# Kernel tuning notes

Hardware: AMD Instinct MI355X
Metric: run time of the kernel (lower is better)

The kernel has to match this reference:

```python
import jax, jax.numpy as jnp
import numpy as np

L_IN, L_FREQ, L_OUT = 128, 64, 64
C_IN, C_OUT, T_DIM = 64, 64, 256
SPIN = 1

# ---------- self-contained spin-weighted SHT (MW sampling), replacing s2fft ----------

def _mw_thetas(L, extended):
    n = 2 * L - 1 if extended else L
    return (2 * np.arange(n) + 1) * np.pi / (2 * L - 1)

def _wigner_d_stack(L, thetas, n):
    # d^l_{m,n}(theta) = <l,m| exp(-i theta Jy) |l,n>, computed via eigh of the
    # Hermitian angular-momentum operator Jy. Output (ntheta, L, 2L-1), m at col L-1+m.
    nth = len(thetas)
    out = np.zeros((nth, L, 2 * L - 1), dtype=np.float64)
    for l in range(abs(n), L):
        dim = 2 * l + 1
        m = np.arange(-l, l).astype(np.float64)
        ap = np.sqrt(l * (l + 1.0) - m * (m + 1.0))
        Jy = np.zeros((dim, dim), dtype=np.complex128)
        i = np.arange(dim - 1)
        Jy[i + 1, i] = -0.5j * ap
        Jy[i, i + 1] = 0.5j * ap
        lam, V = np.linalg.eigh(Jy)
        coeff = V * np.conj(V[l + n, :])[None, :]
        phases = np.exp(-1j * np.outer(lam, thetas))
        out[:, l, L - 1 - l:L + l] = (coeff @ phases).T.real
    return out

def _mw_quad_weights(L):
    # per-theta weights on the mirror-extended grid: q_t = (1/(2L-1)) sum_k w(k) e^{ik theta_t}
    # with w(k) = int_0^pi e^{ik t} sin(t) dt
    k = np.arange(-(L - 1), L)
    den = np.where(np.abs(k) == 1, 1, 1 - k * k).astype(np.float64)
    w = np.where(k % 2 == 0, 2.0 / den, 0.0).astype(np.complex128)
    w[k == 1] = 0.5j * np.pi
    w[k == -1] = -0.5j * np.pi
    th = _mw_thetas(L, True)
    return ((w[None, :] * np.exp(1j * np.outer(th, k))).sum(1) / (2 * L - 1)).real

# transform kernels are constants (built once at import, numpy)
_D_FWD = jnp.asarray(_wigner_d_stack(L_IN, _mw_thetas(L_IN, True), -SPIN) * _mw_quad_weights(L_IN)[:, None, None], jnp.float32)
_D_INV = jnp.asarray(_wigner_d_stack(L_OUT, _mw_thetas(L_OUT, False), -SPIN), jnp.float32)
_CL_IN = jnp.asarray(((-1.0) ** SPIN) * np.sqrt((2 * np.arange(L_IN) + 1) / (4 * np.pi)), jnp.float32)
_CL_OUT = jnp.asarray(((-1.0) ** SPIN) * np.sqrt((2 * np.arange(L_OUT) + 1) / (4 * np.pi)), jnp.float32)
_m_all = np.arange(-(L_IN - 1), L_IN)
_PARITY = jnp.asarray(np.where((_m_all + SPIN) % 2 == 0, 1.0, -1.0), jnp.float32)

def sht_forward(x):
    # x: (L_IN, 2*L_IN-1, C) real spatial -> flm: (L_IN, 2*L_IN-1, C) complex, m at L_IN-1+m
    nphi = 2 * L_IN - 1
    ftm = jnp.fft.fftshift(jnp.fft.fft(x, axis=1), axes=1) * (2 * jnp.pi / nphi)
    # mirror extension in theta with (-1)^(m+spin) parity (all channels at once)
    g_ext = jnp.concatenate([ftm, _PARITY[None, :, None] * ftm[::-1][1:]], axis=0)
    flm = jnp.einsum('tlm,tmc->lmc', _D_FWD, g_ext)
    return flm * _CL_IN[:, None, None]

def sht_inverse(flm):
    # flm: (L_OUT, 2*L_OUT-1, C) complex -> (L_OUT, 2*L_OUT-1, C) real spatial
    ftm = jnp.einsum('tlm,lmc->tmc', _D_INV, flm * _CL_OUT[:, None, None])
    return (jnp.fft.ifft(jnp.fft.ifftshift(ftm, axes=1), axis=1) * (2 * L_OUT - 1)).real

def resize_flm(flm, l_in, l_out):
    # centered truncation / zero-pad of (L, 2L-1, C) harmonic coefficients
    if l_out <= l_in:
        d = l_in - l_out
        return flm[:l_out, d:d + 2 * l_out - 1]
    d = l_out - l_in
    return jnp.pad(flm, ((0, d), (d, d), (0, 0)))

# ---------- inputs and parameters ----------

def setup_inputs():
    key = jax.random.key(0)
    ks = jax.random.split(key, 12)
    n = lambda i, shape, s: jax.random.normal(ks[i], shape, jnp.float32) * s
    return {
        'x': jax.random.normal(ks[0], (L_IN, 2 * L_IN - 1, C_IN), jnp.float32),
        't_emb': jax.random.normal(ks[1], (T_DIM,), jnp.float32),
        'spec_conv_w': n(2, (C_IN, C_OUT), (1.0 / C_IN) ** 0.5),
        'spec_conv_b': jnp.zeros((C_OUT,), jnp.float32),
        'spec_wr': n(3, (L_FREQ, C_IN, C_OUT), (0.5 / C_IN) ** 0.5),
        'spec_wi': n(4, (L_FREQ, C_IN, C_OUT), (0.5 / C_IN) ** 0.5),
        'spec_tr_w': n(5, (T_DIM, L_FREQ), (1.0 / T_DIM) ** 0.5),
        'spec_tr_b': jnp.zeros((L_FREQ,), jnp.float32),
        'spec_ti_w': n(6, (T_DIM, L_FREQ), (1.0 / T_DIM) ** 0.5),
        'spec_ti_b': jnp.zeros((L_FREQ,), jnp.float32),
        'spat_conv1_w': n(7, (C_IN, C_OUT), (1.0 / C_IN) ** 0.5),
        'spat_conv1_b': jnp.zeros((C_OUT,), jnp.float32),
        'spat_t_w': n(8, (T_DIM, 2 * C_OUT), (1.0 / T_DIM) ** 0.5),
        'spat_t_b': jnp.zeros((2 * C_OUT,), jnp.float32),
        'spat_weight': n(9, (C_OUT, C_OUT), 0.01),
        'spat_conv2_w': n(10, (C_OUT, C_OUT), (1.0 / C_OUT) ** 0.5),
        'spat_conv2_b': jnp.zeros((C_OUT,), jnp.float32),
        'ln_scale': jnp.ones((C_OUT,), jnp.float32),
        'ln_bias': jnp.zeros((C_OUT,), jnp.float32),
    }

def reference(x, t_emb, spec_conv_w, spec_conv_b, spec_wr, spec_wi, spec_tr_w, spec_tr_b, spec_ti_w, spec_ti_b, spat_conv1_w, spat_conv1_b, spat_t_w, spat_t_b, spat_weight, spat_conv2_w, spat_conv2_b, ln_scale, ln_bias):
    # ----- SphericalSpectralTimeConv branch -----
    flm = sht_forward(x)                                   # (L_IN, 2L_IN-1, C_IN) complex
    flm = resize_flm(flm, L_IN, L_FREQ)                    # (L_FREQ, 2L_FREQ-1, C_IN)
    conv_flm = jnp.einsum('lmi,io->lmo', flm, spec_conv_w) + spec_conv_b
    t_c = (t_emb @ spec_tr_w + spec_tr_b) + 1j * (t_emb @ spec_ti_w + spec_ti_b)   # (L_FREQ,)
    w = t_c[:, None, None] * (spec_wr + 1j * spec_wi)      # (L_FREQ, C_IN, C_OUT)
    flm = jnp.einsum('lmi,lio->lmo', flm, w) + conv_flm
    xs = sht_inverse(resize_flm(flm, L_FREQ, L_OUT))       # (L_OUT, 2L_OUT-1, C_OUT) real
    xs = xs / (jnp.linalg.norm(xs, axis=-1, keepdims=True) + 1e-6)
    # ----- SpatialTimeConv branch (path='down') -----
    h = jnp.einsum('lmi,io->lmo', x, spat_conv1_w) + spat_conv1_b
    t = t_emb @ spat_t_w + spat_t_b
    w_t, b_t = t[:C_OUT], t[C_OUT:]
    h = jnp.einsum('lmi,io->lmo', h, w_t[None, :] * spat_weight)
    h = sht_inverse(resize_flm(sht_forward(h), L_IN, L_OUT))
    h = jnp.einsum('lmi,io->lmo', h, spat_conv2_w) + spat_conv2_b + b_t
    # ----- combine: add, gelu, LayerNorm (eps=1e-6 over channels) -----
    y = jax.nn.gelu(xs + h)
    mu = jnp.mean(y, axis=-1, keepdims=True)
    var = jnp.var(y, axis=-1, keepdims=True)
    return (y - mu) * jax.lax.rsqrt(var + 1e-6) * ln_scale + ln_bias
```

## Files before the change

### kernel.cpp

```cpp
#include <hip/hip_runtime.h>
#include <math.h>

#define DPI 3.141592653589793238462643383279502884

__device__ __forceinline__ float wave_sum64(float v) {
#pragma unroll
  for (int off = 32; off > 0; off >>= 1) v += __shfl_xor(v, off, 64);
  return v;
}

__device__ __forceinline__ float gelu_tanh(float v) {
  float u = 0.7978845608028654f * (v + 0.044715f * v * v * v);
  return 0.5f * v * (1.0f + tanhf(u));
}

#define CN255F ((float)(-2.0 * DPI / 255.0))
#define CN127F ((float)(2.0 * DPI / 127.0))


__device__ __forceinline__ void dft_block(int idx, int tid, const float* __restrict__ x,
                                          float* __restrict__ Are, float* __restrict__ Aim,
                                          float* __restrict__ Bre, float* __restrict__ Bim,
                                          char* sm) {
  float* xs_ = (float*)sm;
  int t = idx >> 1, ph = idx & 1;
  float* ore = ph ? Bre : Are;
  float* oim = ph ? Bim : Aim;
  int pbase = ph * 128;
  int Ktot = ph ? 127 : 128;
  int cg_ = tid & 15, mg = tid >> 4;
  float wr[4], wi[4], rc[4], rs[4];
#pragma unroll
  for (int j = 0; j < 4; ++j) {
    int m = mg * 4 + j;
    __sincosf(CN255F * (float)m, &rs[j], &rc[j]);
    int r0 = (m * pbase) % 255;
    __sincosf(CN255F * (float)r0, &wi[j], &wr[j]);
  }
  float accr[4][4], acci[4][4];
#pragma unroll
  for (int j = 0; j < 4; ++j)
#pragma unroll
    for (int q = 0; q < 4; ++q) { accr[j][q] = 0.f; acci[j][q] = 0.f; }
  for (int k0 = 0; k0 < Ktot; k0 += 64) {
    int kn = (Ktot - k0 < 64) ? Ktot - k0 : 64;
    __syncthreads();
    {
      const float4* src = (const float4*)(x + ((size_t)t * 255 + pbase + k0) * 64);
      float4* dst = (float4*)xs_;
      int lim = kn * 16;
#pragma unroll
      for (int q = 0; q < 4; ++q) {
        int fidx = tid + q * 256;
        if (fidx < lim) dst[fidx] = src[fidx];
      }
    }
    __syncthreads();
#pragma unroll 2
    for (int k = 0; k < kn; ++k) {
      float4 xv = *(const float4*)&xs_[k * 64 + cg_ * 4];
      float xv4[4] = {xv.x, xv.y, xv.z, xv.w};
#pragma unroll
      for (int j = 0; j < 4; ++j) {
#pragma unroll
        for (int q = 0; q < 4; ++q) {
          accr[j][q] = fmaf(xv4[q], wr[j], accr[j][q]);
          acci[j][q] = fmaf(xv4[q], wi[j], acci[j][q]);
        }
        float nw = wr[j] * rc[j] - wi[j] * rs[j];
        wi[j] = fmaf(wr[j], rs[j], wi[j] * rc[j]);
        wr[j] = nw;
      }
    }
  }
#pragma unroll
  for (int j = 0; j < 4; ++j) {
    int mi = mg * 4 + j;
    size_t ob = ((size_t)t * 64 + mi) * 64 + cg_ * 4;
    *(float4*)(ore + ob) = make_float4(accr[j][0], accr[j][1], accr[j][2], accr[j][3]);
    *(float4*)(oim + ob) = make_float4(acci[j][0], acci[j][1], acci[j][2], acci[j][3]);
  }
}

__device__ __forceinline__ void wigner_block(int wb, int tid, float* __restrict__ Deff,
                                             float* __restrict__ Dinv, char* sm) {
  float* LF = (float*)sm;
  double* red = (double*)(sm + 512);
  float* clf = (float*)(sm + 1024);
  int mode = (wb < 128) ? 0 : 1;
  int t, mm;
  if (mode == 0) { t = wb; mm = tid; }
  else { mm = wb - 128; t = (tid < 64) ? tid : 63; }
  if (tid < 64) clf[tid] = (float)(-sqrt((2.0 * tid + 1.0) / (4.0 * DPI)));
  if (tid < 128) LF[tid] = (tid == 0) ? 0.f : logf((float)tid);
  __syncthreads();
  for (int s = 1; s < 128; s <<= 1) {
    float add = (tid < 128 && tid >= s) ? LF[tid - s] : 0.f;
    __syncthreads();
    if (tid < 128) LF[tid] += add;
    __syncthreads();
  }
  double denomN = (mode == 0) ? 255.0 : 127.0;
  double beta = (2.0 * t + 1.0) * DPI / denomN;
  float coeff = 1.0f;
  if (mode == 0) {
    if (tid < 63) {
      int k = 2 * (tid + 1);
      red[tid] = 8.0 * cos((double)k * beta) / (1.0 - (double)k * (double)k);
    } else if (tid == 63) {
      red[63] = 4.0;
    }
    __syncthreads();
    for (int s = 32; s > 0; s >>= 1) {
      if (tid < s) red[tid] += red[tid + s];
      __syncthreads();
    }
    double s = red[0] / 255.0;
    if (t == 127) s *= 0.5;
    coeff = (float)(s * (2.0 * DPI / 255.0));
  }
  bool active = (mode == 0) ? (tid < 127) : (tid < 64);
  if (!active) return;
  int m = mm - 63;
  double chd, shd;
  sincos(0.5 * beta, &shd, &chd);
  float cbf = (float)cos(beta);
  float chf = (float)chd, shf = (float)shd;
  int am = (m < 0) ? -m : m;
  int l0v = (am > 1) ? am : 1;
  float seed;
  if (m == 0) {
    seed = -1.4142135623730951f * shf * chf;
  } else {
    int j = am;
    float lch = logf(chf), lsh = logf(shf);
    float e0 = 0.5f * (LF[2 * j] - LF[j - 1] - LF[j + 1]);
    float expo = (m >= 1) ? e0 + (float)(j - 1) * lch + (float)(j + 1) * lsh
                          : e0 + (float)(j + 1) * lch + (float)(j - 1) * lsh;
    float sv = __expf(expo);
    seed = (m >= 1 && ((m + 1) & 1)) ? -sv : sv;
  }
  float dl = seed, dm1 = 0.0f, S_cur = 0.0f;
  float mf = (float)m;
  for (int l = 0; l < 64; ++l) {
    float val = 0.0f;
    if (l >= l0v) {
      val = dl * coeff * clf[l];
      float Ld = (float)l, lp = Ld + 1.0f;
      float S_next = sqrtf((lp * lp - mf * mf) * (lp * lp - 1.0f));
      float num1 = (2.0f * Ld + 1.0f) * (Ld * lp * cbf + mf);
      float dn = (num1 * dl - lp * S_cur * dm1) / (Ld * S_next);
      dm1 = dl; dl = dn; S_cur = S_next;
    }
    if (mode == 0) Deff[((size_t)t * 127 + mm) * 64 + l] = val;
    else Dinv[((size_t)mm * 64 + l) * 64 + t] = val;
  }
}

__device__ __forceinline__ void a2_block(int l, int tid, const float* __restrict__ temb,
                                         const float* __restrict__ trw, const float* __restrict__ trb,
                                         const float* __restrict__ tiw, const float* __restrict__ tib,
                                         const float* __restrict__ scw, const float* __restrict__ swr,
                                         const float* __restrict__ swi, float2* __restrict__ A2,
                                         char* sm) {
  float* fb1 = (float*)sm;
  float* fb2 = (float*)(sm + 1024);
  fb1[tid] = temb[tid] * trw[tid * 64 + l];
  fb2[tid] = temb[tid] * tiw[tid * 64 + l];
  __syncthreads();
  for (int s = 128; s > 0; s >>= 1) {
    if (tid < s) { fb1[tid] += fb1[tid + s]; fb2[tid] += fb2[tid + s]; }
    __syncthreads();
  }
  float tr = fb1[0] + trb[l], ti = fb2[0] + tib[l];
  int o = tid & 63, iq = tid >> 6;
  for (int i = iq * 16; i < iq * 16 + 16; ++i) {
    int idx = (l * 64 + i) * 64 + o;
    float r = swr[idx], s2 = swi[idx];
    A2[idx] = make_float2(scw[i * 64 + o] + tr * r - ti * s2, tr * s2 + ti * r);
  }
}

__device__ __forceinline__ void m_block(int j, int tid, const float* __restrict__ temb,
                                        const float* __restrict__ stw, const float* __restrict__ stb,
                                        const float* __restrict__ c1w, const float* __restrict__ c1b,
                                        const float* __restrict__ sweight, float* __restrict__ Mm,
                                        float* __restrict__ bias2, char* sm) {
  float* fb1 = (float*)sm;
  float* fb2 = (float*)(sm + 1024);
  int o = tid & 63, part = tid >> 6;
  float p = 0.f;
  for (int k = part * 64; k < part * 64 + 64; ++k)
    p = fmaf(temb[k], stw[k * 128 + o], p);
  fb1[part * 64 + o] = p;
  __syncthreads();
  if (part == 0) fb2[o] = fb1[o] + fb1[64 + o] + fb1[128 + o] + fb1[192 + o] + stb[o];
  __syncthreads();
  float tvo = fb2[o];
  float q = 0.f;
  for (int i = part * 16; i < part * 16 + 16; ++i)
    q = fmaf(c1w[j * 64 + i], sweight[i * 64 + o], q);
  __syncthreads();
  fb1[part * 64 + o] = q;
  __syncthreads();
  if (part == 0) Mm[j * 64 + o] = tvo * (fb1[o] + fb1[64 + o] + fb1[128 + o] + fb1[192 + o]);
  if (j == 0) {
    float bq = 0.f;
    for (int i = part * 16; i < part * 16 + 16; ++i)
      bq = fmaf(c1b[i], sweight[i * 64 + o], bq);
    __syncthreads();
    fb1[part * 64 + o] = bq;
    __syncthreads();
    if (part == 0) bias2[o] = tvo * (fb1[o] + fb1[64 + o] + fb1[128 + o] + fb1[192 + o]);
  }
}

__device__ __forceinline__ void tv_block(int tid, const float* __restrict__ temb,
                                         const float* __restrict__ stw, const float* __restrict__ stb,
                                         float* __restrict__ tv, char* sm) {
  float* fb1 = (float*)sm;
  int o = tid & 127, part = tid >> 7;
  float p = 0.f;
  for (int k = part * 128; k < part * 128 + 128; ++k)
    p = fmaf(temb[k], stw[k * 128 + o], p);
  fb1[part * 128 + o] = p;
  __syncthreads();
  if (part == 0) tv[o] = fb1[o] + fb1[128 + o] + stb[o];
}

__global__ __launch_bounds__(256) void ct_pre(
    const float* __restrict__ x, const float* __restrict__ temb,
    const float* __restrict__ trw, const float* __restrict__ trb,
    const float* __restrict__ tiw, const float* __restrict__ tib,
    const float* __restrict__ stw, const float* __restrict__ stb,
    const float* __restrict__ scw, const float* __restrict__ swr,
    const float* __restrict__ swi, const float* __restrict__ c1w,
    const float* __restrict__ c1b, const float* __restrict__ sweight,
    float* __restrict__ Deff, float* __restrict__ Dinv,
    float2* __restrict__ A2, float* __restrict__ Mm,
    float* __restrict__ bias2, float* __restrict__ tv,
    float* __restrict__ ftmA_re, float* __restrict__ ftmA_im,
    float* __restrict__ ftmB_re, float* __restrict__ ftmB_im) {
  __shared__ __align__(16) char sm[16384];
  int vb = blockIdx.x;
  int tid = threadIdx.x;
  if (vb < 255) wigner_block(vb, tid, Deff, Dinv, sm);
  else if (vb < 319) a2_block(vb - 255, tid, temb, trw, trb, tiw, tib, scw, swr, swi, A2, sm);
  else if (vb < 383) m_block(vb - 319, tid, temb, stw, stb, c1w, c1b, sweight, Mm, bias2, sm);
  else if (vb < 384) tv_block(tid, temb, stw, stb, tv, sm);
  else dft_block(vb - 384, tid, x, ftmA_re, ftmA_im, ftmB_re, ftmB_im, sm);
}

__global__ __launch_bounds__(256) void ct_projf(const float* __restrict__ Deff,
                                                const float* __restrict__ fAre,
                                                const float* __restrict__ fAim,
                                                const float* __restrict__ fBre,
                                                const float* __restrict__ fBim,
                                                float* __restrict__ flmA_re, float* __restrict__ flmA_im,
                                                float* __restrict__ flmB_re, float* __restrict__ flmB_im) {
  __shared__ float Dsh[64][32];
  __shared__ float fr_[64][64], fi_[64][64];
  int mm = blockIdx.x, lh = blockIdx.y, th = blockIdx.z;
  float* ore = th ? flmB_re : flmA_re;
  float* oim = th ? flmB_im : flmA_im;
  int tb = th * 64;
  int mi = (mm >= 63) ? (mm - 63) : (63 - mm);
  float csign = (mm >= 63) ? 1.0f : -1.0f;
  int tid = threadIdx.x;
  int cg_ = tid & 15, lg = tid >> 4;
  for (int e = tid; e < 64 * 32; e += 256) {
    int r = e >> 5, li = e & 31;
    Dsh[r][li] = Deff[((size_t)(tb + r) * 127 + mm) * 64 + lh * 32 + li];
  }
  for (int e = tid; e < 64 * 64; e += 256) {
    int r = e >> 6, c = e & 63;
    size_t idx = ((size_t)(tb + r) * 64 + mi) * 64 + c;
    fr_[r][c] = fAre[idx] + fBre[idx];
    fi_[r][c] = csign * (fAim[idx] + fBim[idx]);
  }
  __syncthreads();
  float ar[2][4], ai[2][4];
#pragma unroll
  for (int li = 0; li < 2; ++li)
#pragma unroll
    for (int q = 0; q < 4; ++q) { ar[li][q] = 0.f; ai[li][q] = 0.f; }
#pragma unroll 4
  for (int k = 0; k < 64; ++k) {
    float4 fr4 = *(const float4*)&fr_[k][cg_ * 4];
    float4 fi4 = *(const float4*)&fi_[k][cg_ * 4];
    float2 d2 = *(const float2*)&Dsh[k][lg * 2];
    float frv[4] = {fr4.x, fr4.y, fr4.z, fr4.w};
    float fiv[4] = {fi4.x, fi4.y, fi4.z, fi4.w};
    float dv[2] = {d2.x, d2.y};
#pragma unroll
    for (int li = 0; li < 2; ++li)
#pragma unroll
      for (int q = 0; q < 4; ++q) {
        ar[li][q] = fmaf(dv[li], frv[q], ar[li][q]);
        ai[li][q] = fmaf(dv[li], fiv[q], ai[li][q]);
      }
  }
#pragma unroll
  for (int li = 0; li < 2; ++li) {
    size_t row = ((size_t)mm * 64 + lh * 32 + lg * 2 + li) * 64 + cg_ * 4;
    *(float4*)(ore + row) = make_float4(ar[li][0], ar[li][1], ar[li][2], ar[li][3]);
    *(float4*)(oim + row) = make_float4(ai[li][0], ai[li][1], ai[li][2], ai[li][3]);
  }
}

__global__ __launch_bounds__(256) void ct_mix(const float* __restrict__ flmA_re,
                                              const float* __restrict__ flmA_im,
                                              const float* __restrict__ flmB_re,
                                              const float* __restrict__ flmB_im,
                                              const float2* __restrict__ A2,
                                              const float* __restrict__ Mm,
                                              const float* __restrict__ scb,
                                              const float* __restrict__ bias2,
                                              const float* __restrict__ Deff,
                                              float* __restrict__ s_re, float* __restrict__ s_im,
                                              float* __restrict__ h_re, float* __restrict__ h_im) {
  __shared__ float Ar_[64][32], Ai_[64][32], Msh[64][32];
  __shared__ float Br_[64][65], Bi_[64][65];
  __shared__ float rb[256];
  int l = blockIdx.x, mh = blockIdx.y, oh = blockIdx.z;
  int tid = threadIdx.x;
  int og = tid & 15, mg = tid >> 4;
  rb[tid] = (mh == 0 && tid < 128) ? Deff[((size_t)tid * 127 + 63) * 64 + l] : 0.f;
  __syncthreads();
  for (int s = 128; s > 0; s >>= 1) {
    if (tid < s) rb[tid] += rb[tid + s];
    __syncthreads();
  }
  float slv = rb[0];
  for (int e = tid; e < 64 * 32; e += 256) {
    int r = e >> 5, oi = e & 31;
    float2 aa = A2[((size_t)l * 64 + r) * 64 + oh * 32 + oi];
    Ar_[r][oi] = aa.x; Ai_[r][oi] = aa.y;
    Msh[r][oi] = Mm[r * 64 + oh * 32 + oi];
  }
  for (int e = tid; e < 64 * 64; e += 256) {
    int mi = e >> 6, i = e & 63;
    int gmm = mh * 64 + mi; if (gmm > 126) gmm = 126;
    size_t idx = ((size_t)gmm * 64 + l) * 64 + i;
    Br_[mi][i] = flmA_re[idx] + flmB_re[idx];
    Bi_[mi][i] = flmA_im[idx] + flmB_im[idx];
  }
  __syncthreads();
  int o0 = oh * 32 + og * 2;
  float b0[2] = {scb[o0], scb[o0 + 1]};
  float sr[4][2], si[4][2], hr[4][2], hi[4][2];
#pragma unroll
  for (int jm = 0; jm < 4; ++jm)
#pragma unroll
    for (int qo = 0; qo < 2; ++qo) {
      sr[jm][qo] = b0[qo]; si[jm][qo] = 0.f; hr[jm][qo] = 0.f; hi[jm][qo] = 0.f;
    }
#pragma unroll 4
  for (int k = 0; k < 64; ++k) {
    float2 ar2 = *(const float2*)&Ar_[k][og * 2];
    float2 ai2 = *(const float2*)&Ai_[k][og * 2];
    float2 mv2 = *(const float2*)&Msh[k][og * 2];
    float br4[4], bi4[4];
#pragma unroll
    for (int jm = 0; jm < 4; ++jm) {
      br4[jm] = Br_[mg * 4 + jm][k];
      bi4[jm] = Bi_[mg * 4 + jm][k];
    }
    float arv[2] = {ar2.x, ar2.y}, aiv[2] = {ai2.x, ai2.y}, mvv[2] = {mv2.x, mv2.y};
#pragma unroll
    for (int jm = 0; jm < 4; ++jm)
#pragma unroll
      for (int qo = 0; qo < 2; ++qo) {
        sr[jm][qo] = fmaf(br4[jm], arv[qo], sr[jm][qo]);
        sr[jm][qo] = fmaf(-bi4[jm], aiv[qo], sr[jm][qo]);
        si[jm][qo] = fmaf(br4[jm], aiv[qo], si[jm][qo]);
        si[jm][qo] = fmaf(bi4[jm], arv[qo], si[jm][qo]);
        hr[jm][qo] = fmaf(br4[jm], mvv[qo], hr[jm][qo]);
        hi[jm][qo] = fmaf(bi4[jm], mvv[qo], hi[jm][qo]);
      }
  }
  float bb[2] = {bias2[o0], bias2[o0 + 1]};
#pragma unroll
  for (int jm = 0; jm < 4; ++jm) {
    int gmm = mh * 64 + mg * 4 + jm;
    if (gmm > 126) continue;
    if (gmm == 63) {
#pragma unroll
      for (int qo = 0; qo < 2; ++qo)
        hr[jm][qo] = fmaf(255.0f * slv, bb[qo], hr[jm][qo]);
    }
    size_t row = ((size_t)gmm * 64 + l) * 64 + o0;
    *(float2*)(s_re + row) = make_float2(sr[jm][0], sr[jm][1]);
    *(float2*)(s_im + row) = make_float2(si[jm][0], si[jm][1]);
    *(float2*)(h_re + row) = make_float2(hr[jm][0], hr[jm][1]);
    *(float2*)(h_im + row) = make_float2(hi[jm][0], hi[jm][1]);
  }
}

__global__ __launch_bounds__(256) void ct_proji(const float* __restrict__ Dinv,
                                                const float* __restrict__ s_re,
                                                const float* __restrict__ s_im,
                                                const float* __restrict__ h_re,
                                                const float* __restrict__ h_im,
                                                float* __restrict__ fos_re, float* __restrict__ fos_im,
                                                float* __restrict__ foh_re, float* __restrict__ foh_im) {
  __shared__ float Dsh[64][64];
  __shared__ float Br_[64][32], Bi_[64][32];
  int mm = blockIdx.x, br = blockIdx.y, ch = blockIdx.z;
  const float* ire = br ? h_re : s_re;
  const float* iim = br ? h_im : s_im;
  float* ore = br ? foh_re : fos_re;
  float* oim = br ? foh_im : fos_im;
  int tid = threadIdx.x;
  int cg_ = tid & 15, tg = tid >> 4;
  for (int e = tid; e < 64 * 64; e += 256) {
    int r = e >> 6, tt = e & 63;
    Dsh[r][tt] = Dinv[((size_t)mm * 64 + r) * 64 + tt];
  }
  for (int e = tid; e < 64 * 32; e += 256) {
    int r = e >> 5, cc = e & 31;
    size_t idx = ((size_t)mm * 64 + r) * 64 + ch * 32 + cc;
    Br_[r][cc] = ire[idx];
    Bi_[r][cc] = iim[idx];
  }
  __syncthreads();
  float ar[4][2], ai[4][2];
#pragma unroll
  for (int j = 0; j < 4; ++j)
#pragma unroll
    for (int q = 0; q < 2; ++q) { ar[j][q] = 0.f; ai[j][q] = 0.f; }
#pragma unroll 4
  for (int k = 0; k < 64; ++k) {
    float4 d4 = *(const float4*)&Dsh[k][tg * 4];
    float2 fr2 = *(const float2*)&Br_[k][cg_ * 2];
    float2 fi2 = *(const float2*)&Bi_[k][cg_ * 2];
    float dv[4] = {d4.x, d4.y, d4.z, d4.w};
    float frv[2] = {fr2.x, fr2.y}, fiv[2] = {fi2.x, fi2.y};
#pragma unroll
    for (int j = 0; j < 4; ++j)
#pragma unroll
      for (int q = 0; q < 2; ++q) {
        ar[j][q] = fmaf(dv[j], frv[q], ar[j][q]);
        ai[j][q] = fmaf(dv[j], fiv[q], ai[j][q]);
      }
  }
#pragma unroll
  for (int j = 0; j < 4; ++j) {
    int t = tg * 4 + j;
    size_t ob = ((size_t)t * 127 + mm) * 64 + ch * 32 + cg_ * 2;
    *(float2*)(ore + ob) = make_float2(ar[j][0], ar[j][1]);
    *(float2*)(oim + ob) = make_float2(ai[j][0], ai[j][1]);
  }
}

__global__ __launch_bounds__(256) void ct_idft(const float* __restrict__ fos_re,
                                               const float* __restrict__ fos_im,
                                               const float* __restrict__ foh_re,
                                               const float* __restrict__ foh_im,
                                               float* __restrict__ xsbA, float* __restrict__ xsbB,
                                               float* __restrict__ hsbA, float* __restrict__ hsbB) {
  __shared__ float Br_[32][64], Bi_[32][64];
  int t = blockIdx.x, br = blockIdx.y;
  int z = blockIdx.z;
  int ph = z >> 1, kh = z & 1;
  const float* fre = br ? foh_re : fos_re;
  const float* fim = br ? foh_im : fos_im;
  float* outp = br ? (kh ? hsbB : hsbA) : (kh ? xsbB : xsbA);
  int kbase = kh * 64;
  int Ktot = kh ? 63 : 64;
  int tid = threadIdx.x;
  int cg_ = tid & 15, pg = tid >> 4;
  float wc[4], ws[4], rc[4], rs[4];
#pragma unroll
  for (int j = 0; j < 4; ++j) {
    int gp = ph * 64 + pg * 4 + j; if (gp > 126) gp = 126;
    __sincosf(CN127F * (float)gp, &rs[j], &rc[j]);
    int r0 = ((kbase - 63) * gp) % 127;
    __sincosf(CN127F * (float)r0, &ws[j], &wc[j]);
  }
  float acc[4][4];
#pragma unroll
  for (int j = 0; j < 4; ++j)
#pragma unroll
    for (int q = 0; q < 4; ++q) acc[j][q] = 0.f;
  for (int k0 = 0; k0 < Ktot; k0 += 32) {
    int kn = (Ktot - k0 < 32) ? Ktot - k0 : 32;
    __syncthreads();
    for (int e = tid; e < 32 * 64; e += 256) {
      int r = e >> 6, j = e & 63;
      if (r < kn) {
        size_t bidx = ((size_t)t * 127 + kbase + k0 + r) * 64 + j;
        Br_[r][j] = fre[bidx]; Bi_[r][j] = fim[bidx];
      }
    }
    __syncthreads();
#pragma unroll 2
    for (int k = 0; k < kn; ++k) {
      float4 b_r = *(const float4*)&Br_[k][cg_ * 4];
      float4 b_i = *(const float4*)&Bi_[k][cg_ * 4];
      float brv[4] = {b_r.x, b_r.y, b_r.z, b_r.w};
      float biv[4] = {b_i.x, b_i.y, b_i.z, b_i.w};
#pragma unroll
      for (int j = 0; j < 4; ++j) {
#pragma unroll
        for (int q = 0; q < 4; ++q) {
          acc[j][q] = fmaf(brv[q], wc[j], acc[j][q]);
          acc[j][q] = fmaf(biv[q], -ws[j], acc[j][q]);
        }
        float nw = wc[j] * rc[j] - ws[j] * rs[j];
        ws[j] = fmaf(wc[j], rs[j], ws[j] * rc[j]);
        wc[j] = nw;
      }
    }
  }
#pragma unroll
  for (int j = 0; j < 4; ++j) {
    int gp = ph * 64 + pg * 4 + j;
    if (gp > 126) continue;
    *(float4*)(outp + ((size_t)t * 127 + gp) * 64 + cg_ * 4) =
        make_float4(acc[j][0], acc[j][1], acc[j][2], acc[j][3]);
  }
}

__global__ __launch_bounds__(256) void ct_fin(const float* __restrict__ xsbA,
                                              const float* __restrict__ xsbB,
                                              const float* __restrict__ hsbA,
                                              const float* __restrict__ hsbB,
                                              const float* __restrict__ c2w,
                                              const float* __restrict__ c2b,
                                              const float* __restrict__ tv,
                                              const float* __restrict__ lns,
                                              const float* __restrict__ lnb,
                                              float* __restrict__ out) {
  int w = threadIdx.x >> 6, lane = threadIdx.x & 63;
  size_t row = (size_t)blockIdx.x * 4 + w;
  size_t base = row * 64 + lane;
  float hv = hsbA[base] + hsbB[base];
  float xv = xsbA[base] + xsbB[base];
  float acc = c2b[lane] + tv[64 + lane];
#pragma unroll 16
  for (int i = 0; i < 64; ++i)
    acc = fmaf(__shfl(hv, i, 64), c2w[i * 64 + lane], acc);
  float ss = wave_sum64(xv * xv);
  xv = xv / (sqrtf(ss) + 1e-6f);
  float y = xv + acc;
  float g = gelu_tanh(y);
  float mu = wave_sum64(g) * (1.0f / 64.0f);
  float d = g - mu;
  float var = wave_sum64(d * d) * (1.0f / 64.0f);
  out[base] = d * rsqrtf(var + 1e-6f) * lns[lane] + lnb[lane];
}

extern "C" void kernel_launch(void* const* d_in, const int* in_sizes, int n_in,
                              void* d_out, int out_size, void* d_ws, size_t ws_size,
                              hipStream_t stream) {
  const float* x = (const float*)d_in[0];
  const float* temb = (const float*)d_in[1];
  const float* scw = (const float*)d_in[2];
  const float* scb = (const float*)d_in[3];
  const float* swr = (const float*)d_in[4];
  const float* swi = (const float*)d_in[5];
  const float* strw = (const float*)d_in[6];
  const float* strb = (const float*)d_in[7];
  const float* stiw = (const float*)d_in[8];
  const float* stib = (const float*)d_in[9];
  const float* c1w = (const float*)d_in[10];
  const float* c1b = (const float*)d_in[11];
  const float* stw = (const float*)d_in[12];
  const float* stb = (const float*)d_in[13];
  const float* sweight = (const float*)d_in[14];
  const float* c2w = (const float*)d_in[15];
  const float* c2b = (const float*)d_in[16];
  const float* lns = (const float*)d_in[17];
  const float* lnb = (const float*)d_in[18];
  float* out = (float*)d_out;

  char* base = (char*)d_ws;
  size_t off = 0;
  auto alloc = [&](size_t bytes) -> void* {
    void* p = base + off;
    off += (bytes + 255) & ~(size_t)255;
    return p;
  };
  float* tv = (float*)alloc(128 * sizeof(float));
  float* Mm = (float*)alloc(4096 * sizeof(float));
  float* bias2 = (float*)alloc(64 * sizeof(float));
  float2* A2 = (float2*)alloc(262144 * sizeof(float2));
  float* Deff = (float*)alloc(1040384 * sizeof(float));
  float* Dinv = (float*)alloc(520192 * sizeof(float));
  float* ftmA_re = (float*)alloc(524288 * sizeof(float));
  float* ftmA_im = (float*)alloc(524288 * sizeof(float));
  float* ftmB_re = (float*)alloc(524288 * sizeof(float));
  float* ftmB_im = (float*)alloc(524288 * sizeof(float));
  float* flmA_re = (float*)alloc(520192 * sizeof(float));
  float* flmA_im = (float*)alloc(520192 * sizeof(float));
  float* flmB_re = (float*)alloc(520192 * sizeof(float));
  float* flmB_im = (float*)alloc(520192 * sizeof(float));
  if (off > ws_size) return;
  float* s_re = ftmA_re;
  float* s_im = ftmA_im;
  float* h_re = ftmB_re;
  float* h_im = ftmB_im;
  float* fos_re = Deff;
  float* fos_im = Deff + 520192;
  float* foh_re = flmA_re;
  float* foh_im = flmA_im;
  float* xsbA = flmB_re;
  float* xsbB = flmB_im;
  float* hsbA = ftmA_re;
  float* hsbB = ftmA_im;

  hipLaunchKernelGGL(ct_pre, dim3(640), dim3(256), 0, stream,
                     x, temb, strw, strb, stiw, stib, stw, stb,
                     scw, swr, swi, c1w, c1b, sweight,
                     Deff, Dinv, A2, Mm, bias2, tv,
                     ftmA_re, ftmA_im, ftmB_re, ftmB_im);
  hipLaunchKernelGGL(ct_projf, dim3(127, 2, 2), dim3(256), 0, stream, Deff,
                     ftmA_re, ftmA_im, ftmB_re, ftmB_im,
                     flmA_re, flmA_im, flmB_re, flmB_im);
  hipLaunchKernelGGL(ct_mix, dim3(64, 2, 2), dim3(256), 0, stream,
                     flmA_re, flmA_im, flmB_re, flmB_im, A2, Mm, scb, bias2, Deff,
                     s_re, s_im, h_re, h_im);
  hipLaunchKernelGGL(ct_proji, dim3(127, 2, 2), dim3(256), 0, stream, Dinv,
                     s_re, s_im, h_re, h_im, fos_re, fos_im, foh_re, foh_im);
  hipLaunchKernelGGL(ct_idft, dim3(64, 2, 4), dim3(256), 0, stream,
                     fos_re, fos_im, foh_re, foh_im, xsbA, xsbB, hsbA, hsbB);
  hipLaunchKernelGGL(ct_fin, dim3(2032), dim3(256), 0, stream, xsbA, xsbB, hsbA, hsbB,
                     c2w, c2b, tv, lns, lnb, out);
}
```

Before: 193.8 us.

## Remove split-K partial sums across DFT, projection and IDFT stages

Drops the two-way split-K scheme in the forward DFT, forward Wigner projection and inverse DFT, so each block walks the full reduction and writes a single output instead of partials that later kernels add together. This halves the intermediate buffers and the extra loads and adds in consumers, and gives every buffer its own workspace allocation instead of aliasing. The DFT blocks are moved to the front of the fused prologue grid, and the quadrature weight sum is done in float with an exact integer angle reduction instead of double. In exchange the grids get fewer, longer blocks, which lowers parallelism on a large GPU.

After: 195.4 us. About the same (+0.8%).

```diff
diff --git a/kernel.cpp b/kernel.cpp
--- a/kernel.cpp
+++ b/kernel.cpp
@@ -16,37 +16,31 @@
 
 #define CN255F ((float)(-2.0 * DPI / 255.0))
 #define CN127F ((float)(2.0 * DPI / 127.0))
-
-
-__device__ __forceinline__ void dft_block(int idx, int tid, const float* __restrict__ x,
-                                          float* __restrict__ Are, float* __restrict__ Aim,
-                                          float* __restrict__ Bre, float* __restrict__ Bim,
+#define PIO255F ((float)(DPI / 255.0))
+
+
+__device__ __forceinline__ void dft_block(int t, int tid, const float* __restrict__ x,
+                                          float* __restrict__ ftm_re, float* __restrict__ ftm_im,
                                           char* sm) {
   float* xs_ = (float*)sm;
-  int t = idx >> 1, ph = idx & 1;
-  float* ore = ph ? Bre : Are;
-  float* oim = ph ? Bim : Aim;
-  int pbase = ph * 128;
-  int Ktot = ph ? 127 : 128;
   int cg_ = tid & 15, mg = tid >> 4;
   float wr[4], wi[4], rc[4], rs[4];
 #pragma unroll
   for (int j = 0; j < 4; ++j) {
     int m = mg * 4 + j;
     __sincosf(CN255F * (float)m, &rs[j], &rc[j]);
-    int r0 = (m * pbase) % 255;
-    __sincosf(CN255F * (float)r0, &wi[j], &wr[j]);
+    wr[j] = 1.0f; wi[j] = 0.0f;
   }
   float accr[4][4], acci[4][4];
 #pragma unroll
   for (int j = 0; j < 4; ++j)
 #pragma unroll
     for (int q = 0; q < 4; ++q) { accr[j][q] = 0.f; acci[j][q] = 0.f; }
-  for (int k0 = 0; k0 < Ktot; k0 += 64) {
-    int kn = (Ktot - k0 < 64) ? Ktot - k0 : 64;
+  for (int k0 = 0; k0 < 255; k0 += 64) {
+    int kn = (255 - k0 < 64) ? 255 - k0 : 64;
     __syncthreads();
     {
-      const float4* src = (const float4*)(x + ((size_t)t * 255 + pbase + k0) * 64);
+      const float4* src = (const float4*)(x + ((size_t)t * 255 + k0) * 64);
       float4* dst = (float4*)xs_;
       int lim = kn * 16;
 #pragma unroll
@@ -77,15 +71,15 @@
   for (int j = 0; j < 4; ++j) {
     int mi = mg * 4 + j;
     size_t ob = ((size_t)t * 64 + mi) * 64 + cg_ * 4;
-    *(float4*)(ore + ob) = make_float4(accr[j][0], accr[j][1], accr[j][2], accr[j][3]);
-    *(float4*)(oim + ob) = make_float4(acci[j][0], acci[j][1], acci[j][2], acci[j][3]);
+    *(float4*)(ftm_re + ob) = make_float4(accr[j][0], accr[j][1], accr[j][2], accr[j][3]);
+    *(float4*)(ftm_im + ob) = make_float4(acci[j][0], acci[j][1], acci[j][2], acci[j][3]);
   }
 }
 
 __device__ __forceinline__ void wigner_block(int wb, int tid, float* __restrict__ Deff,
                                              float* __restrict__ Dinv, char* sm) {
   float* LF = (float*)sm;
-  double* red = (double*)(sm + 512);
+  float* red = (float*)(sm + 512);
   float* clf = (float*)(sm + 1024);
   int mode = (wb < 128) ? 0 : 1;
   int t, mm;
@@ -100,28 +94,31 @@
     if (tid < 128) LF[tid] += add;
     __syncthreads();
   }
-  double denomN = (mode == 0) ? 255.0 : 127.0;
-  double beta = (2.0 * t + 1.0) * DPI / denomN;
   float coeff = 1.0f;
+  int odd = 2 * t + 1;
   if (mode == 0) {
     if (tid < 63) {
       int k = 2 * (tid + 1);
-      red[tid] = 8.0 * cos((double)k * beta) / (1.0 - (double)k * (double)k);
+      int e = (k * odd) % 510;
+      float ang = (float)e * PIO255F;
+      red[tid] = 8.0f * __cosf(ang) / (1.0f - (float)(k * k));
     } else if (tid == 63) {
-      red[63] = 4.0;
+      red[63] = 4.0f;
     }
     __syncthreads();
     for (int s = 32; s > 0; s >>= 1) {
       if (tid < s) red[tid] += red[tid + s];
       __syncthreads();
     }
-    double s = red[0] / 255.0;
-    if (t == 127) s *= 0.5;
-    coeff = (float)(s * (2.0 * DPI / 255.0));
+    float s = red[0] / 255.0f;
+    if (t == 127) s *= 0.5f;
+    coeff = s * (float)(2.0 * DPI / 255.0);
   }
   bool active = (mode == 0) ? (tid < 127) : (tid < 64);
   if (!active) return;
   int m = mm - 63;
+  double denomN = (mode == 0) ? 255.0 : 127.0;
+  double beta = (double)odd * DPI / denomN;
   double chd, shd;
   sincos(0.5 * beta, &shd, &chd);
   float cbf = (float)cos(beta);
@@ -239,79 +236,75 @@
     float* __restrict__ Deff, float* __restrict__ Dinv,
     float2* __restrict__ A2, float* __restrict__ Mm,
     float* __restrict__ bias2, float* __restrict__ tv,
-    float* __restrict__ ftmA_re, float* __restrict__ ftmA_im,
-    float* __restrict__ ftmB_re, float* __restrict__ ftmB_im) {
+    float* __restrict__ ftm_re, float* __restrict__ ftm_im) {
   __shared__ __align__(16) char sm[16384];
   int vb = blockIdx.x;
   int tid = threadIdx.x;
-  if (vb < 255) wigner_block(vb, tid, Deff, Dinv, sm);
-  else if (vb < 319) a2_block(vb - 255, tid, temb, trw, trb, tiw, tib, scw, swr, swi, A2, sm);
-  else if (vb < 383) m_block(vb - 319, tid, temb, stw, stb, c1w, c1b, sweight, Mm, bias2, sm);
-  else if (vb < 384) tv_block(tid, temb, stw, stb, tv, sm);
-  else dft_block(vb - 384, tid, x, ftmA_re, ftmA_im, ftmB_re, ftmB_im, sm);
+  if (vb < 128) dft_block(vb, tid, x, ftm_re, ftm_im, sm);
+  else if (vb < 383) wigner_block(vb - 128, tid, Deff, Dinv, sm);
+  else if (vb < 447) a2_block(vb - 383, tid, temb, trw, trb, tiw, tib, scw, swr, swi, A2, sm);
+  else if (vb < 511) m_block(vb - 447, tid, temb, stw, stb, c1w, c1b, sweight, Mm, bias2, sm);
+  else tv_block(tid, temb, stw, stb, tv, sm);
 }
 
 __global__ __launch_bounds__(256) void ct_projf(const float* __restrict__ Deff,
-                                                const float* __restrict__ fAre,
-                                                const float* __restrict__ fAim,
-                                                const float* __restrict__ fBre,
-                                                const float* __restrict__ fBim,
-                                                float* __restrict__ flmA_re, float* __restrict__ flmA_im,
-                                                float* __restrict__ flmB_re, float* __restrict__ flmB_im) {
+                                                const float* __restrict__ ftm_re,
+                                                const float* __restrict__ ftm_im,
+                                                float* __restrict__ flm_re,
+                                                float* __restrict__ flm_im) {
   __shared__ float Dsh[64][32];
   __shared__ float fr_[64][64], fi_[64][64];
-  int mm = blockIdx.x, lh = blockIdx.y, th = blockIdx.z;
-  float* ore = th ? flmB_re : flmA_re;
-  float* oim = th ? flmB_im : flmA_im;
-  int tb = th * 64;
+  int mm = blockIdx.x, lh = blockIdx.y;
   int mi = (mm >= 63) ? (mm - 63) : (63 - mm);
   float csign = (mm >= 63) ? 1.0f : -1.0f;
   int tid = threadIdx.x;
   int cg_ = tid & 15, lg = tid >> 4;
-  for (int e = tid; e < 64 * 32; e += 256) {
-    int r = e >> 5, li = e & 31;
-    Dsh[r][li] = Deff[((size_t)(tb + r) * 127 + mm) * 64 + lh * 32 + li];
-  }
-  for (int e = tid; e < 64 * 64; e += 256) {
-    int r = e >> 6, c = e & 63;
-    size_t idx = ((size_t)(tb + r) * 64 + mi) * 64 + c;
-    fr_[r][c] = fAre[idx] + fBre[idx];
-    fi_[r][c] = csign * (fAim[idx] + fBim[idx]);
-  }
-  __syncthreads();
   float ar[2][4], ai[2][4];
 #pragma unroll
   for (int li = 0; li < 2; ++li)
 #pragma unroll
     for (int q = 0; q < 4; ++q) { ar[li][q] = 0.f; ai[li][q] = 0.f; }
+  for (int th2 = 0; th2 < 2; ++th2) {
+    int tb = th2 * 64;
+    __syncthreads();
+    for (int e = tid; e < 64 * 32; e += 256) {
+      int r = e >> 5, li = e & 31;
+      Dsh[r][li] = Deff[((size_t)(tb + r) * 127 + mm) * 64 + lh * 32 + li];
+    }
+    for (int e = tid; e < 64 * 64; e += 256) {
+      int r = e >> 6, c = e & 63;
+      size_t idx = ((size_t)(tb + r) * 64 + mi) * 64 + c;
+      fr_[r][c] = ftm_re[idx];
+      fi_[r][c] = csign * ftm_im[idx];
+    }
+    __syncthreads();
 #pragma unroll 4
-  for (int k = 0; k < 64; ++k) {
-    float4 fr4 = *(const float4*)&fr_[k][cg_ * 4];
-    float4 fi4 = *(const float4*)&fi_[k][cg_ * 4];
-    float2 d2 = *(const float2*)&Dsh[k][lg * 2];
-    float frv[4] = {fr4.x, fr4.y, fr4.z, fr4.w};
-    float fiv[4] = {fi4.x, fi4.y, fi4.z, fi4.w};
-    float dv[2] = {d2.x, d2.y};
-#pragma unroll
-    for (int li = 0; li < 2; ++li)
-#pragma unroll
-      for (int q = 0; q < 4; ++q) {
-        ar[li][q] = fmaf(dv[li], frv[q], ar[li][q]);
-        ai[li][q] = fmaf(dv[li], fiv[q], ai[li][q]);
-      }
+    for (int k = 0; k < 64; ++k) {
+      float4 fr4 = *(const float4*)&fr_[k][cg_ * 4];
+      float4 fi4 = *(const float4*)&fi_[k][cg_ * 4];
+      float2 d2 = *(const float2*)&Dsh[k][lg * 2];
+      float frv[4] = {fr4.x, fr4.y, fr4.z, fr4.w};
+      float fiv[4] = {fi4.x, fi4.y, fi4.z, fi4.w};
+      float dv[2] = {d2.x, d2.y};
+#pragma unroll
+      for (int li = 0; li < 2; ++li)
+#pragma unroll
+        for (int q = 0; q < 4; ++q) {
+          ar[li][q] = fmaf(dv[li], frv[q], ar[li][q]);
+          ai[li][q] = fmaf(dv[li], fiv[q], ai[li][q]);
+        }
+    }
   }
 #pragma unroll
   for (int li = 0; li < 2; ++li) {
     size_t row = ((size_t)mm * 64 + lh * 32 + lg * 2 + li) * 64 + cg_ * 4;
-    *(float4*)(ore + row) = make_float4(ar[li][0], ar[li][1], ar[li][2], ar[li][3]);
-    *(float4*)(oim + row) = make_float4(ai[li][0], ai[li][1], ai[li][2], ai[li][3]);
-  }
-}
-
-__global__ __launch_bounds__(256) void ct_mix(const float* __restrict__ flmA_re,
-                                              const float* __restrict__ flmA_im,
-                                              const float* __restrict__ flmB_re,
-                                              const float* __restrict__ flmB_im,
+    *(float4*)(flm_re + row) = make_float4(ar[li][0], ar[li][1], ar[li][2], ar[li][3]);
+    *(float4*)(flm_im + row) = make_float4(ai[li][0], ai[li][1], ai[li][2], ai[li][3]);
+  }
+}
+
+__global__ __launch_bounds__(256) void ct_mix(const float* __restrict__ flm_re,
+                                              const float* __restrict__ flm_im,
                                               const float2* __restrict__ A2,
                                               const float* __restrict__ Mm,
                                               const float* __restrict__ scb,
@@ -342,8 +335,8 @@
     int mi = e >> 6, i = e & 63;
     int gmm = mh * 64 + mi; if (gmm > 126) gmm = 126;
     size_t idx = ((size_t)gmm * 64 + l) * 64 + i;
-    Br_[mi][i] = flmA_re[idx] + flmB_re[idx];
-    Bi_[mi][i] = flmA_im[idx] + flmB_im[idx];
+    Br_[mi][i] = flm_re[idx];
+    Bi_[mi][i] = flm_im[idx];
   }
   __syncthreads();
   int o0 = oh * 32 + og * 2;
@@ -457,17 +450,12 @@
                                                const float* __restrict__ fos_im,
                                                const float* __restrict__ foh_re,
                                                const float* __restrict__ foh_im,
-                                               float* __restrict__ xsbA, float* __restrict__ xsbB,
-                                               float* __restrict__ hsbA, float* __restrict__ hsbB) {
+                                               float* __restrict__ xsb, float* __restrict__ hsb) {
   __shared__ float Br_[32][64], Bi_[32][64];
-  int t = blockIdx.x, br = blockIdx.y;
-  int z = blockIdx.z;
-  int ph = z >> 1, kh = z & 1;
+  int t = blockIdx.x, br = blockIdx.y, ph = blockIdx.z;
   const float* fre = br ? foh_re : fos_re;
   const float* fim = br ? foh_im : fos_im;
-  float* outp = br ? (kh ? hsbB : hsbA) : (kh ? xsbB : xsbA);
-  int kbase = kh * 64;
-  int Ktot = kh ? 63 : 64;
+  float* outp = br ? hsb : xsb;
   int tid = threadIdx.x;
   int cg_ = tid & 15, pg = tid >> 4;
   float wc[4], ws[4], rc[4], rs[4];
@@ -475,7 +463,7 @@
   for (int j = 0; j < 4; ++j) {
     int gp = ph * 64 + pg * 4 + j; if (gp > 126) gp = 126;
     __sincosf(CN127F * (float)gp, &rs[j], &rc[j]);
-    int r0 = ((kbase - 63) * gp) % 127;
+    int r0 = (-63 * gp) % 127;
     __sincosf(CN127F * (float)r0, &ws[j], &wc[j]);
   }
   float acc[4][4];
@@ -483,13 +471,13 @@
   for (int j = 0; j < 4; ++j)
 #pragma unroll
     for (int q = 0; q < 4; ++q) acc[j][q] = 0.f;
-  for (int k0 = 0; k0 < Ktot; k0 += 32) {
-    int kn = (Ktot - k0 < 32) ? Ktot - k0 : 32;
+  for (int k0 = 0; k0 < 127; k0 += 32) {
+    int kn = (127 - k0 < 32) ? 127 - k0 : 32;
     __syncthreads();
     for (int e = tid; e < 32 * 64; e += 256) {
       int r = e >> 6, j = e & 63;
       if (r < kn) {
-        size_t bidx = ((size_t)t * 127 + kbase + k0 + r) * 64 + j;
+        size_t bidx = ((size_t)t * 127 + k0 + r) * 64 + j;
         Br_[r][j] = fre[bidx]; Bi_[r][j] = fim[bidx];
       }
     }
@@ -522,10 +510,8 @@
   }
 }
 
-__global__ __launch_bounds__(256) void ct_fin(const float* __restrict__ xsbA,
-                                              const float* __restrict__ xsbB,
-                                              const float* __restrict__ hsbA,
-                                              const float* __restrict__ hsbB,
+__global__ __launch_bounds__(256) void ct_fin(const float* __restrict__ xsb,
+                                              const float* __restrict__ hsb,
                                               const float* __restrict__ c2w,
                                               const float* __restrict__ c2b,
                                               const float* __restrict__ tv,
@@ -535,8 +521,8 @@
   int w = threadIdx.x >> 6, lane = threadIdx.x & 63;
   size_t row = (size_t)blockIdx.x * 4 + w;
   size_t base = row * 64 + lane;
-  float hv = hsbA[base] + hsbB[base];
-  float xv = xsbA[base] + xsbB[base];
+  float hv = hsb[base];
+  float xv = xsb[base];
   float acc = c2b[lane] + tv[64 + lane];
 #pragma unroll 16
   for (int i = 0; i < 64; ++i)
@@ -588,43 +574,35 @@
   float2* A2 = (float2*)alloc(262144 * sizeof(float2));
   float* Deff = (float*)alloc(1040384 * sizeof(float));
   float* Dinv = (float*)alloc(520192 * sizeof(float));
-  float* ftmA_re = (float*)alloc(524288 * sizeof(float));
-  float* ftmA_im = (float*)alloc(524288 * sizeof(float));
-  float* ftmB_re = (float*)alloc(524288 * sizeof(float));
-  float* ftmB_im = (float*)alloc(524288 * sizeof(float));
-  float* flmA_re = (float*)alloc(520192 * sizeof(float));
-  float* flmA_im = (float*)alloc(520192 * sizeof(float));
-  float* flmB_re = (float*)alloc(520192 * sizeof(float));
-  float* flmB_im = (float*)alloc(520192 * sizeof(float));
+  float* ftm_re = (float*)alloc(524288 * sizeof(float));
+  float* ftm_im = (float*)alloc(524288 * sizeof(float));
+  float* flm_re = (float*)alloc(520192 * sizeof(float));
+  float* flm_im = (float*)alloc(520192 * sizeof(float));
+  float* s_re = (float*)alloc(520192 * sizeof(float));
+  float* s_im = (float*)alloc(520192 * sizeof(float));
+  float* h_re = (float*)alloc(520192 * sizeof(float));
+  float* h_im = (float*)alloc(520192 * sizeof(float));
+  float* fos_re = (float*)alloc(520192 * sizeof(float));
+  float* fos_im = (float*)alloc(520192 * sizeof(float));
+  float* foh_re = (float*)alloc(520192 * sizeof(float));
+  float* foh_im = (float*)alloc(520192 * sizeof(float));
+  float* xsb = (float*)alloc(520192 * sizeof(float));
+  float* hsb = (float*)alloc(520192 * sizeof(float));
   if (off > ws_size) return;
-  float* s_re = ftmA_re;
-  float* s_im = ftmA_im;
-  float* h_re = ftmB_re;
-  float* h_im = ftmB_im;
-  float* fos_re = Deff;
-  float* fos_im = Deff + 520192;
-  float* foh_re = flmA_re;
-  float* foh_im = flmA_im;
-  float* xsbA = flmB_re;
-  float* xsbB = flmB_im;
-  float* hsbA = ftmA_re;
-  float* hsbB = ftmA_im;
-
-  hipLaunchKernelGGL(ct_pre, dim3(640), dim3(256), 0, stream,
+
+  hipLaunchKernelGGL(ct_pre, dim3(512), dim3(256), 0, stream,
                      x, temb, strw, strb, stiw, stib, stw, stb,
                      scw, swr, swi, c1w, c1b, sweight,
-                     Deff, Dinv, A2, Mm, bias2, tv,
-                     ftmA_re, ftmA_im, ftmB_re, ftmB_im);
-  hipLaunchKernelGGL(ct_projf, dim3(127, 2, 2), dim3(256), 0, stream, Deff,
-                     ftmA_re, ftmA_im, ftmB_re, ftmB_im,
-                     flmA_re, flmA_im, flmB_re, flmB_im);
+                     Deff, Dinv, A2, Mm, bias2, tv, ftm_re, ftm_im);
+  hipLaunchKernelGGL(ct_projf, dim3(127, 2), dim3(256), 0, stream, Deff,
+                     ftm_re, ftm_im, flm_re, flm_im);
   hipLaunchKernelGGL(ct_mix, dim3(64, 2, 2), dim3(256), 0, stream,
-                     flmA_re, flmA_im, flmB_re, flmB_im, A2, Mm, scb, bias2, Deff,
+                     flm_re, flm_im, A2, Mm, scb, bias2, Deff,
                      s_re, s_im, h_re, h_im);
   hipLaunchKernelGGL(ct_proji, dim3(127, 2, 2), dim3(256), 0, stream, Dinv,
                      s_re, s_im, h_re, h_im, fos_re, fos_im, foh_re, foh_im);
-  hipLaunchKernelGGL(ct_idft, dim3(64, 2, 4), dim3(256), 0, stream,
-                     fos_re, fos_im, foh_re, foh_im, xsbA, xsbB, hsbA, hsbB);
-  hipLaunchKernelGGL(ct_fin, dim3(2032), dim3(256), 0, stream, xsbA, xsbB, hsbA, hsbB,
+  hipLaunchKernelGGL(ct_idft, dim3(64, 2, 2), dim3(256), 0, stream,
+                     fos_re, fos_im, foh_re, foh_im, xsb, hsb);
+  hipLaunchKernelGGL(ct_fin, dim3(2032), dim3(256), 0, stream, xsb, hsb,
                      c2w, c2b, tv, lns, lnb, out);
 }
```
